# Performance work log

Measured on AMD Instinct MI355X. Metric: run time of the kernel, lower is better.

## Reference

```python
import jax, jax.numpy as jnp
import numpy as np

N = 40000          # nodes
E = 640000         # edges (before self-loops)
G = 64             # graphs
EMBED_DIM = 128
GAT_HIDDEN = 64    # per-head channels for g1/g2
GAT_OUT_DIM = 64   # per-head channels for g3 (concat=False)
HEADS = (4, 4, 4)
NEG_SLOPE = 0.2


def setup_inputs() -> dict:
    key = jax.random.key(0)
    ks = jax.random.split(key, 16)
    x = jax.random.normal(ks[0], (N, EMBED_DIM), dtype=jnp.float32)
    edge_index = jax.random.randint(ks[1], (2, E), 0, N, dtype=jnp.int64)
    batch = jnp.sort(jax.random.randint(ks[2], (N,), 0, G, dtype=jnp.int64))

    def lin(k, i, o):
        return jax.random.normal(k, (i, o), dtype=jnp.float32) * (1.0 / np.sqrt(i))

    H1, H2, H3 = HEADS
    d1_in, d1_out = EMBED_DIM, GAT_HIDDEN
    d2_in, d2_out = GAT_HIDDEN * H1, GAT_HIDDEN
    d3_in, d3_out = GAT_HIDDEN * H2, GAT_OUT_DIM
    params = dict(
        Wl1=lin(ks[3], d1_in, H1 * d1_out), Wr1=lin(ks[4], d1_in, H1 * d1_out),
        att1=jax.random.normal(ks[5], (H1, d1_out), dtype=jnp.float32) * 0.1,
        b1=jnp.zeros((H1 * d1_out,), jnp.float32),
        Wl2=lin(ks[6], d2_in, H2 * d2_out), Wr2=lin(ks[7], d2_in, H2 * d2_out),
        att2=jax.random.normal(ks[8], (H2, d2_out), dtype=jnp.float32) * 0.1,
        b2=jnp.zeros((H2 * d2_out,), jnp.float32),
        Wl3=lin(ks[9], d3_in, H3 * d3_out), Wr3=lin(ks[10], d3_in, H3 * d3_out),
        att3=jax.random.normal(ks[11], (H3, d3_out), dtype=jnp.float32) * 0.1,
        b3=jnp.zeros((d3_out,), jnp.float32),
        Wc=lin(ks[12], GAT_OUT_DIM, 2), bc=jnp.zeros((2,), jnp.float32),
    )
    return dict(x=x, edge_index=edge_index, batch=batch, **params)


def _gatv2(x, src, dst, Wl, Wr, att, bias, heads, out_c, concat):
    n = x.shape[0]
    xl = (x @ Wl).reshape(n, heads, out_c)   # source transform
    xr = (x @ Wr).reshape(n, heads, out_c)   # target transform
    # per-edge GATv2 score: att . LeakyReLU(xl[j] + xr[i])
    e = jax.nn.leaky_relu(xl[src] + xr[dst], NEG_SLOPE)      # [E,H,C]
    score = jnp.einsum('ehc,hc->eh', e, att)                  # [E,H]
    # segment softmax over incoming edges of each target node
    smax = jax.ops.segment_max(score, dst, num_segments=n)
    escore = jnp.exp(score - smax[dst])
    denom = jax.ops.segment_sum(escore, dst, num_segments=n)
    alpha = escore / (denom[dst] + 1e-16)                     # [E,H]
    out = jax.ops.segment_sum(alpha[:, :, None] * xl[src], dst, num_segments=n)
    out = out.reshape(n, heads * out_c) if concat else out.mean(axis=1)
    return out + bias


def reference(x, edge_index, batch, Wl1, Wr1, att1, b1, Wl2, Wr2, att2, b2,
              Wl3, Wr3, att3, b3, Wc, bc):
    n = x.shape[0]
    loops = jnp.arange(n, dtype=edge_index.dtype)
    src = jnp.concatenate([edge_index[0], loops])  # add self-loops (PyG default)
    dst = jnp.concatenate([edge_index[1], loops])
    act = lambda h: jax.nn.leaky_relu(h, NEG_SLOPE)
    h = act(_gatv2(x, src, dst, Wl1, Wr1, att1, b1, HEADS[0], GAT_HIDDEN, True))
    h = act(_gatv2(h, src, dst, Wl2, Wr2, att2, b2, HEADS[1], GAT_HIDDEN, True))
    h = _gatv2(h, src, dst, Wl3, Wr3, att3, b3, HEADS[2], GAT_OUT_DIM, False)
    g = jax.ops.segment_max(h, batch, num_segments=G)  # global_max_pool
    logits = g @ Wc + bc
    return logits, g
```

## Files before the change

### kernel.cpp

```cpp
#include <hip/hip_runtime.h>
#include <cstdint>

#define NN 40000
#define EE 640000
#define GG 64

typedef short bf16x8 __attribute__((ext_vector_type(8)));
typedef float f32x4 __attribute__((ext_vector_type(4)));

__device__ __forceinline__ float lrelu(float x) { return x > 0.f ? x : 0.2f * x; }

__device__ __forceinline__ unsigned short f2bf(float f) {
    unsigned u = __float_as_uint(f);
    return (unsigned short)((u + 0x7FFFu + ((u >> 16) & 1u)) >> 16);
}
__device__ __forceinline__ float bf2f(unsigned short h) {
    return __uint_as_float(((unsigned)h) << 16);
}

__device__ __forceinline__ unsigned fenc(float x) {
    unsigned u = __float_as_uint(x);
    return (u & 0x80000000u) ? ~u : (u | 0x80000000u);
}
__device__ __forceinline__ float fdec(unsigned e) {
    unsigned u = (e & 0x80000000u) ? (e ^ 0x80000000u) : ~e;
    return __uint_as_float(u);
}
#define ENC_NEG_INF 0x007FFFFFu

__device__ __forceinline__ void gload16(const void* g, void* l) {
    __builtin_amdgcn_global_load_lds(
        (const __attribute__((address_space(1))) unsigned int*)g,
        (__attribute__((address_space(3))) unsigned int*)l,
        16, 0, 0);
}

__global__ void k_init(int* deg, unsigned* gmax) {
    int i = blockIdx.x * blockDim.x + threadIdx.x;
    if (i < NN) deg[i] = 0;
    if (i < GG * 64) gmax[i] = ENC_NEG_INF;
}

__global__ void k_count(const int* __restrict__ dst, int* deg) {
    int e = blockIdx.x * blockDim.x + threadIdx.x;
    if (e < EE) atomicAdd(&deg[dst[e]], 1);
}

#define SCAN_T 1024
__global__ __launch_bounds__(SCAN_T) void k_scan(const int* __restrict__ deg,
                                                 int* row_ptr, int* cursor) {
    __shared__ int part[SCAN_T];
    const int t = threadIdx.x;
    const int CH = (NN + SCAN_T - 1) / SCAN_T;
    const int base = t * CH;
    int s = 0;
    for (int j = 0; j < CH; ++j) {
        int idx = base + j;
        if (idx < NN) s += deg[idx];
    }
    part[t] = s;
    __syncthreads();
    for (int off = 1; off < SCAN_T; off <<= 1) {
        int v = (t >= off) ? part[t - off] : 0;
        __syncthreads();
        part[t] += v;
        __syncthreads();
    }
    int run = (t == 0) ? 0 : part[t - 1];
    for (int j = 0; j < CH; ++j) {
        int idx = base + j;
        if (idx < NN) {
            row_ptr[idx] = run;
            cursor[idx]  = run;
            run += deg[idx];
        }
    }
    if (t == SCAN_T - 1) row_ptr[NN] = run;
}

__global__ void k_scatter(const int* __restrict__ src, const int* __restrict__ dst,
                          int* cursor, int* csr_src) {
    int e = blockIdx.x * blockDim.x + threadIdx.x;
    if (e < EE) {
        int p = atomicAdd(&cursor[dst[e]], 1);
        csr_src[p] = src[e];
    }
}

__global__ void k_xsplit(const float* __restrict__ x,
                         ushort* __restrict__ ah, ushort* __restrict__ am, int total4) {
    int i = blockIdx.x * blockDim.x + threadIdx.x;
    if (i >= total4) return;
    float4 v = ((const float4*)x)[i];
    ushort4 H, M;
    float* pv = &v.x;
    unsigned short* pH = &H.x; unsigned short* pM = &M.x;
#pragma unroll
    for (int j = 0; j < 4; ++j) {
        float a = pv[j];
        unsigned short h = f2bf(a);
        pH[j] = h;
        pM[j] = f2bf(a - bf2f(h));
    }
    ((ushort4*)ah)[i] = H;
    ((ushort4*)am)[i] = M;
}

__global__ __launch_bounds__(256) void k_wsplit(const float* __restrict__ W, int K,
                                                ushort* __restrict__ th,
                                                ushort* __restrict__ tm) {
    __shared__ float t[32][33];
    const int n0 = blockIdx.x * 32;
    const int k0 = blockIdx.y * 32;
    const int tx = threadIdx.x;
    const int ty = threadIdx.y;
#pragma unroll
    for (int i = 0; i < 4; ++i) {
        int kl = ty * 4 + i;
        t[kl][tx] = W[(size_t)(k0 + kl) * 256 + n0 + tx];
    }
    __syncthreads();
#pragma unroll
    for (int i = 0; i < 4; ++i) {
        int nl = ty * 4 + i;
        float a = t[tx][nl];
        unsigned short h = f2bf(a);
        size_t o = (size_t)(n0 + nl) * K + k0 + tx;
        th[o] = h;
        tm[o] = f2bf(a - bf2f(h));
    }
}

#define GBM 128
#define GBK 32
__global__ __launch_bounds__(256, 2) void gemm2(const ushort* __restrict__ Ah,
                                                const ushort* __restrict__ Am,
                                                const ushort* __restrict__ Bh,
                                                const ushort* __restrict__ Bm,
                                                float* __restrict__ C,
                                                int M, int K) {
    __shared__ ushort sAh[GBM * GBK];
    __shared__ ushort sAm[GBM * GBK];
    __shared__ ushort sBh[GBM * GBK];
    __shared__ ushort sBm[GBM * GBK];
    const int tid  = threadIdx.x;
    const int lane = tid & 63;
    const int wv   = tid >> 6;
    const int wm   = wv & 1;
    const int wn   = wv >> 1;
    const int bm   = blockIdx.x * GBM;
    const int bn   = blockIdx.y * 128;

    const ushort* gsrc = (wv == 0) ? Ah : (wv == 1) ? Am : (wv == 2) ? Bh : Bm;
    ushort* lbase = (wv == 0) ? sAh : (wv == 1) ? sAm : (wv == 2) ? sBh : sBm;
    const int rowbase = (wv < 2) ? bm : bn;

    f32x4 acc[4][4];
#pragma unroll
    for (int i = 0; i < 4; ++i)
#pragma unroll
        for (int j = 0; j < 4; ++j)
            acc[i][j] = (f32x4){0.f, 0.f, 0.f, 0.f};

    const int rl = lane >> 2;
    const int cs = lane & 3;
    const int fc = lane >> 4;
    const int fr = lane & 15;

    for (int k0 = 0; k0 < K; k0 += GBK) {
#pragma unroll
        for (int j = 0; j < 8; ++j) {
            const int lrow = j * 16 + rl;
            const int c    = cs ^ ((lrow >> 1) & 3);
            int grow = rowbase + lrow;
            grow = (grow >= M) ? (M - 1) : grow;
            gload16(gsrc + (size_t)grow * K + k0 + c * 8, lbase + j * 512);
        }
        __syncthreads();

        bf16x8 aH[4], aM[4], bH[4], bM[4];
#pragma unroll
        for (int mi = 0; mi < 4; ++mi) {
            const int row = wm * 64 + mi * 16 + fr;
            const int idx = row * 32 + (fc ^ ((row >> 1) & 3)) * 8;
            aH[mi] = *(const bf16x8*)&sAh[idx];
            aM[mi] = *(const bf16x8*)&sAm[idx];
        }
#pragma unroll
        for (int ni = 0; ni < 4; ++ni) {
            const int row = wn * 64 + ni * 16 + fr;
            const int idx = row * 32 + (fc ^ ((row >> 1) & 3)) * 8;
            bH[ni] = *(const bf16x8*)&sBh[idx];
            bM[ni] = *(const bf16x8*)&sBm[idx];
        }

#pragma unroll
        for (int mi = 0; mi < 4; ++mi)
#pragma unroll
            for (int ni = 0; ni < 4; ++ni) {
                f32x4 c0 = acc[mi][ni];
                c0 = __builtin_amdgcn_mfma_f32_16x16x32_bf16(aH[mi], bH[ni], c0, 0, 0, 0);
                c0 = __builtin_amdgcn_mfma_f32_16x16x32_bf16(aH[mi], bM[ni], c0, 0, 0, 0);
                c0 = __builtin_amdgcn_mfma_f32_16x16x32_bf16(aM[mi], bH[ni], c0, 0, 0, 0);
                acc[mi][ni] = c0;
            }
        __syncthreads();
    }

#pragma unroll
    for (int mi = 0; mi < 4; ++mi) {
#pragma unroll
        for (int r = 0; r < 4; ++r) {
            const int row = bm + wm * 64 + mi * 16 + (lane >> 4) * 4 + r;
            if (row < M) {
#pragma unroll
                for (int ni = 0; ni < 4; ++ni) {
                    const int col = bn + wn * 64 + ni * 16 + (lane & 15);
                    C[(size_t)row * 256 + col] = acc[mi][ni][r];
                }
            }
        }
    }
}

template <int MODE>
__global__ __launch_bounds__(256) void k_aggregate(const float* __restrict__ xl,
                                                   const float* __restrict__ xr,
                                                   const float* __restrict__ att,
                                                   const float* __restrict__ bias,
                                                   const int* __restrict__ row_ptr,
                                                   const int* __restrict__ csr_src,
                                                   ushort* __restrict__ oh,
                                                   ushort* __restrict__ om,
                                                   float* __restrict__ of) {
    const int wave = threadIdx.x >> 6;
    const int lane = threadIdx.x & 63;
    const int node = blockIdx.x * 4 + wave;
    if (node >= NN) return;

    const float4 xri = ((const float4*)(xr + (size_t)node * 256))[lane];
    const float4 av  = ((const float4*)att)[lane];

    float m = -INFINITY, d = 0.f;
    float a0 = 0.f, a1 = 0.f, a2 = 0.f, a3 = 0.f;

    const int start = row_ptr[node];
    const int endp  = row_ptr[node + 1];
    const int L = endp - start + 1;

    int i = 0;
    for (; i + 4 <= L; i += 4) {
        const int e0 = start + i;
        const int s0 = (e0     < endp) ? csr_src[e0]     : node;
        const int s1 = (e0 + 1 < endp) ? csr_src[e0 + 1] : node;
        const int s2 = (e0 + 2 < endp) ? csr_src[e0 + 2] : node;
        const int s3 = (e0 + 3 < endp) ? csr_src[e0 + 3] : node;
        const float4 x0 = ((const float4*)(xl + (size_t)s0 * 256))[lane];
        const float4 x1 = ((const float4*)(xl + (size_t)s1 * 256))[lane];
        const float4 x2 = ((const float4*)(xl + (size_t)s2 * 256))[lane];
        const float4 x3 = ((const float4*)(xl + (size_t)s3 * 256))[lane];
        float p0 = av.x * lrelu(x0.x + xri.x) + av.y * lrelu(x0.y + xri.y)
                 + av.z * lrelu(x0.z + xri.z) + av.w * lrelu(x0.w + xri.w);
        float p1 = av.x * lrelu(x1.x + xri.x) + av.y * lrelu(x1.y + xri.y)
                 + av.z * lrelu(x1.z + xri.z) + av.w * lrelu(x1.w + xri.w);
        float p2 = av.x * lrelu(x2.x + xri.x) + av.y * lrelu(x2.y + xri.y)
                 + av.z * lrelu(x2.z + xri.z) + av.w * lrelu(x2.w + xri.w);
        float p3 = av.x * lrelu(x3.x + xri.x) + av.y * lrelu(x3.y + xri.y)
                 + av.z * lrelu(x3.z + xri.z) + av.w * lrelu(x3.w + xri.w);
        p0 += __shfl_xor(p0, 1); p1 += __shfl_xor(p1, 1);
        p2 += __shfl_xor(p2, 1); p3 += __shfl_xor(p3, 1);
        p0 += __shfl_xor(p0, 2); p1 += __shfl_xor(p1, 2);
        p2 += __shfl_xor(p2, 2); p3 += __shfl_xor(p3, 2);
        p0 += __shfl_xor(p0, 4); p1 += __shfl_xor(p1, 4);
        p2 += __shfl_xor(p2, 4); p3 += __shfl_xor(p3, 4);
        p0 += __shfl_xor(p0, 8); p1 += __shfl_xor(p1, 8);
        p2 += __shfl_xor(p2, 8); p3 += __shfl_xor(p3, 8);

        const float pm = fmaxf(fmaxf(p0, p1), fmaxf(p2, p3));
        if (__all(pm <= m + 8.f)) {
            const float f0 = __expf(p0 - m), f1 = __expf(p1 - m);
            const float f2 = __expf(p2 - m), f3 = __expf(p3 - m);
            d  += f0 + f1 + f2 + f3;
            a0 += f0 * x0.x + f1 * x1.x + f2 * x2.x + f3 * x3.x;
            a1 += f0 * x0.y + f1 * x1.y + f2 * x2.y + f3 * x3.y;
            a2 += f0 * x0.z + f1 * x1.z + f2 * x2.z + f3 * x3.z;
            a3 += f0 * x0.w + f1 * x1.w + f2 * x2.w + f3 * x3.w;
        } else {
            const float mn = fmaxf(m, pm);
            const float sc = __expf(m - mn);
            const float f0 = __expf(p0 - mn), f1 = __expf(p1 - mn);
            const float f2 = __expf(p2 - mn), f3 = __expf(p3 - mn);
            d  = d  * sc + f0 + f1 + f2 + f3;
            a0 = a0 * sc + f0 * x0.x + f1 * x1.x + f2 * x2.x + f3 * x3.x;
            a1 = a1 * sc + f0 * x0.y + f1 * x1.y + f2 * x2.y + f3 * x3.y;
            a2 = a2 * sc + f0 * x0.z + f1 * x1.z + f2 * x2.z + f3 * x3.z;
            a3 = a3 * sc + f0 * x0.w + f1 * x1.w + f2 * x2.w + f3 * x3.w;
            m = mn;
        }
    }
    for (; i < L; ++i) {
        const int e0 = start + i;
        const int s0 = (e0 < endp) ? csr_src[e0] : node;
        const float4 x0 = ((const float4*)(xl + (size_t)s0 * 256))[lane];
        float p0 = av.x * lrelu(x0.x + xri.x) + av.y * lrelu(x0.y + xri.y)
                 + av.z * lrelu(x0.z + xri.z) + av.w * lrelu(x0.w + xri.w);
        p0 += __shfl_xor(p0, 1);
        p0 += __shfl_xor(p0, 2);
        p0 += __shfl_xor(p0, 4);
        p0 += __shfl_xor(p0, 8);
        if (__all(p0 <= m + 8.f)) {
            const float f0 = __expf(p0 - m);
            d += f0; a0 += f0 * x0.x; a1 += f0 * x0.y; a2 += f0 * x0.z; a3 += f0 * x0.w;
        } else {
            const float mn = fmaxf(m, p0);
            const float sc = __expf(m - mn);
            const float f0 = __expf(p0 - mn);
            d  = d  * sc + f0;
            a0 = a0 * sc + f0 * x0.x;
            a1 = a1 * sc + f0 * x0.y;
            a2 = a2 * sc + f0 * x0.z;
            a3 = a3 * sc + f0 * x0.w;
            m = mn;
        }
    }

    const float inv = 1.f / (d + 1e-16f);
    if (MODE == 0) {
        const int c = lane * 4;
        float v[4];
        v[0] = lrelu(a0 * inv + bias[c + 0]);
        v[1] = lrelu(a1 * inv + bias[c + 1]);
        v[2] = lrelu(a2 * inv + bias[c + 2]);
        v[3] = lrelu(a3 * inv + bias[c + 3]);
        ushort4 H, M4;
        unsigned short* pH = &H.x; unsigned short* pM = &M4.x;
#pragma unroll
        for (int j = 0; j < 4; ++j) {
            unsigned short h = f2bf(v[j]);
            pH[j] = h;
            pM[j] = f2bf(v[j] - bf2f(h));
        }
        const size_t o = (size_t)node * 64 + lane;
        ((ushort4*)oh)[o] = H;
        ((ushort4*)om)[o] = M4;
    } else {
        float v0 = a0 * inv, v1 = a1 * inv, v2 = a2 * inv, v3 = a3 * inv;
        v0 += __shfl_xor(v0, 16); v0 += __shfl_xor(v0, 32);
        v1 += __shfl_xor(v1, 16); v1 += __shfl_xor(v1, 32);
        v2 += __shfl_xor(v2, 16); v2 += __shfl_xor(v2, 32);
        v3 += __shfl_xor(v3, 16); v3 += __shfl_xor(v3, 32);
        if (lane < 16) {
            const int c = lane * 4;
            float4 o;
            o.x = v0 * 0.25f + bias[c + 0];
            o.y = v1 * 0.25f + bias[c + 1];
            o.z = v2 * 0.25f + bias[c + 2];
            o.w = v3 * 0.25f + bias[c + 3];
            ((float4*)(of + (size_t)node * 64))[lane] = o;
        }
    }
}

#define PNB 32
__global__ __launch_bounds__(64) void k_pool(const float* __restrict__ h3,
                                             const int* __restrict__ batch,
                                             unsigned* gmax) {
    const int lane = threadIdx.x;
    const int start = blockIdx.x * PNB;
    if (start >= NN) return;
    const int end = min(start + PNB, NN);
    int curg = batch[start];
    float best = -INFINITY;
    for (int n = start; n < end; ++n) {
        int g = batch[n];
        if (g != curg) {
            atomicMax(&gmax[curg * 64 + lane], fenc(best));
            best = -INFINITY;
            curg = g;
        }
        best = fmaxf(best, h3[(size_t)n * 64 + lane]);
    }
    atomicMax(&gmax[curg * 64 + lane], fenc(best));
}

__global__ void k_decode(const unsigned* __restrict__ gmax, float* __restrict__ outg) {
    int i = blockIdx.x * blockDim.x + threadIdx.x;
    if (i < GG * 64) outg[i] = fdec(gmax[i]);
}

__global__ __launch_bounds__(128) void k_head(const float* __restrict__ g,
                                              const float* __restrict__ Wc,
                                              const float* __restrict__ bc,
                                              float* __restrict__ logits) {
    const int t = threadIdx.x;
    const int gr = t >> 1, o = t & 1;
    float s = bc[o];
    for (int c = 0; c < 64; ++c) s = fmaf(g[gr * 64 + c], Wc[c * 2 + o], s);
    logits[t] = s;
}

extern "C" void kernel_launch(void* const* d_in, const int* in_sizes, int n_in,
                              void* d_out, int out_size, void* d_ws, size_t ws_size,
                              hipStream_t stream) {
    const float* x     = (const float*)d_in[0];
    const int*   ei    = (const int*)d_in[1];
    const int*   batch = (const int*)d_in[2];
    const float* Wl1 = (const float*)d_in[3];
    const float* Wr1 = (const float*)d_in[4];
    const float* att1 = (const float*)d_in[5];
    const float* b1  = (const float*)d_in[6];
    const float* Wl2 = (const float*)d_in[7];
    const float* Wr2 = (const float*)d_in[8];
    const float* att2 = (const float*)d_in[9];
    const float* b2  = (const float*)d_in[10];
    const float* Wl3 = (const float*)d_in[11];
    const float* Wr3 = (const float*)d_in[12];
    const float* att3 = (const float*)d_in[13];
    const float* b3  = (const float*)d_in[14];
    const float* Wc  = (const float*)d_in[15];
    const float* bc  = (const float*)d_in[16];
    float* out = (float*)d_out;

    char* ws = (char*)d_ws;
    size_t off = 0;
    auto alloc = [&](size_t bytes) -> void* {
        void* p = ws + off;
        off += (bytes + 255) & ~(size_t)255;
        return p;
    };
    float*  xlout = (float*)alloc((size_t)NN * 256 * 4);
    float*  xrout = (float*)alloc((size_t)NN * 256 * 4);
    ushort* Ah    = (ushort*)alloc((size_t)NN * 256 * 2);
    ushort* Am    = (ushort*)alloc((size_t)NN * 256 * 2);
    ushort* wt[6][2];
    for (int w = 0; w < 6; ++w)
        for (int s = 0; s < 2; ++s)
            wt[w][s] = (ushort*)alloc((size_t)256 * 256 * 2);
    int*   deg     = (int*)alloc((size_t)NN * 4);
    int*   cursor  = (int*)alloc((size_t)NN * 4);
    int*   row_ptr = (int*)alloc((size_t)(NN + 1) * 4);
    int*   csr_src = (int*)alloc((size_t)EE * 4);
    unsigned* gmax = (unsigned*)alloc((size_t)GG * 64 * 4);
    float* h3 = (float*)Ah;
    if (off > ws_size) return;

    const int* esrc = ei;
    const int* edst = ei + EE;

    k_init<<<(NN + 255) / 256, 256, 0, stream>>>(deg, gmax);
    k_count<<<(EE + 255) / 256, 256, 0, stream>>>(edst, deg);
    k_scan<<<1, SCAN_T, 0, stream>>>(deg, row_ptr, cursor);
    k_scatter<<<(EE + 255) / 256, 256, 0, stream>>>(esrc, edst, cursor, csr_src);

    k_xsplit<<<(NN * 128 / 4 + 255) / 256, 256, 0, stream>>>(x, Ah, Am, NN * 128 / 4);
    const float* Ws[6] = {Wl1, Wr1, Wl2, Wr2, Wl3, Wr3};
    const int    Ks[6] = {128, 128, 256, 256, 256, 256};
    for (int w = 0; w < 6; ++w) {
        dim3 g(8, Ks[w] / 32), b(32, 8);
        k_wsplit<<<g, b, 0, stream>>>(Ws[w], Ks[w], wt[w][0], wt[w][1]);
    }

    const dim3 gg((NN + GBM - 1) / GBM, 2);
    const int agg_blocks = NN / 4;

    gemm2<<<gg, 256, 0, stream>>>(Ah, Am, wt[0][0], wt[0][1], xlout, NN, 128);
    gemm2<<<gg, 256, 0, stream>>>(Ah, Am, wt[1][0], wt[1][1], xrout, NN, 128);
    k_aggregate<0><<<agg_blocks, 256, 0, stream>>>(xlout, xrout, att1, b1, row_ptr, csr_src,
                                                   Ah, Am, nullptr);
    gemm2<<<gg, 256, 0, stream>>>(Ah, Am, wt[2][0], wt[2][1], xlout, NN, 256);
    gemm2<<<gg, 256, 0, stream>>>(Ah, Am, wt[3][0], wt[3][1], xrout, NN, 256);
    k_aggregate<0><<<agg_blocks, 256, 0, stream>>>(xlout, xrout, att2, b2, row_ptr, csr_src,
                                                   Ah, Am, nullptr);
    gemm2<<<gg, 256, 0, stream>>>(Ah, Am, wt[4][0], wt[4][1], xlout, NN, 256);
    gemm2<<<gg, 256, 0, stream>>>(Ah, Am, wt[5][0], wt[5][1], xrout, NN, 256);
    k_aggregate<1><<<agg_blocks, 256, 0, stream>>>(xlout, xrout, att3, b3, row_ptr, csr_src,
                                                   nullptr, nullptr, h3);

    k_pool<<<(NN + PNB - 1) / PNB, 64, 0, stream>>>(h3, batch, gmax);
    k_decode<<<(GG * 64 + 255) / 256, 256, 0, stream>>>(gmax, out + 128);
    k_head<<<1, 128, 0, stream>>>(out + 128, Wc, bc, out);
}
```

Baseline: 721.2 us.

## Fuse left/right GAT projections into one GEMM with double-buffered LDS

Packs Wl and Wr of each layer into one 512-column weight, so a single GEMM produces an interleaved [N,512] xl|xr buffer. This halves the GEMM launches and reads the split activations once per layer instead of twice. The aggregation kernel now gathers source rows and its own target row from the interleaved buffer at a 512-float stride. The GEMM main loop also double-buffers its LDS tiles, prefetching the next K-tile while computing the current one. The cost is twice the shared memory per block, which may reduce occupancy.

```diff
diff --git a/kernel.cpp b/kernel.cpp
--- a/kernel.cpp
+++ b/kernel.cpp
@@ -106,7 +106,7 @@
     ((ushort4*)am)[i] = M;
 }
 
-__global__ __launch_bounds__(256) void k_wsplit(const float* __restrict__ W, int K,
+__global__ __launch_bounds__(256) void k_wsplit(const float* __restrict__ W, int K, int woff,
                                                 ushort* __restrict__ th,
                                                 ushort* __restrict__ tm) {
     __shared__ float t[32][33];
@@ -125,7 +125,7 @@
         int nl = ty * 4 + i;
         float a = t[tx][nl];
         unsigned short h = f2bf(a);
-        size_t o = (size_t)(n0 + nl) * K + k0 + tx;
+        size_t o = (size_t)(woff + n0 + nl) * K + k0 + tx;
         th[o] = h;
         tm[o] = f2bf(a - bf2f(h));
     }
@@ -133,16 +133,16 @@
 
 #define GBM 128
 #define GBK 32
-__global__ __launch_bounds__(256, 2) void gemm2(const ushort* __restrict__ Ah,
-                                                const ushort* __restrict__ Am,
-                                                const ushort* __restrict__ Bh,
-                                                const ushort* __restrict__ Bm,
-                                                float* __restrict__ C,
-                                                int M, int K) {
-    __shared__ ushort sAh[GBM * GBK];
-    __shared__ ushort sAm[GBM * GBK];
-    __shared__ ushort sBh[GBM * GBK];
-    __shared__ ushort sBm[GBM * GBK];
+__global__ __launch_bounds__(256, 2) void gemm2c(const ushort* __restrict__ Ah,
+                                                 const ushort* __restrict__ Am,
+                                                 const ushort* __restrict__ Bh,
+                                                 const ushort* __restrict__ Bm,
+                                                 float* __restrict__ C,
+                                                 int M, int K) {
+    __shared__ ushort sAh[2][GBM * GBK];
+    __shared__ ushort sAm[2][GBM * GBK];
+    __shared__ ushort sBh[2][GBM * GBK];
+    __shared__ ushort sBm[2][GBM * GBK];
     const int tid  = threadIdx.x;
     const int lane = tid & 63;
     const int wv   = tid >> 6;
@@ -152,7 +152,8 @@
     const int bn   = blockIdx.y * 128;
 
     const ushort* gsrc = (wv == 0) ? Ah : (wv == 1) ? Am : (wv == 2) ? Bh : Bm;
-    ushort* lbase = (wv == 0) ? sAh : (wv == 1) ? sAm : (wv == 2) ? sBh : sBm;
+    ushort* l0 = (wv == 0) ? sAh[0] : (wv == 1) ? sAm[0] : (wv == 2) ? sBh[0] : sBm[0];
+    ushort* l1 = (wv == 0) ? sAh[1] : (wv == 1) ? sAm[1] : (wv == 2) ? sBh[1] : sBm[1];
     const int rowbase = (wv < 2) ? bm : bn;
 
     f32x4 acc[4][4];
@@ -167,31 +168,45 @@
     const int fc = lane >> 4;
     const int fr = lane & 15;
 
-    for (int k0 = 0; k0 < K; k0 += GBK) {
+    auto stage = [&](ushort* lb, int kt) {
+        const int k0 = kt * GBK;
 #pragma unroll
         for (int j = 0; j < 8; ++j) {
             const int lrow = j * 16 + rl;
             const int c    = cs ^ ((lrow >> 1) & 3);
             int grow = rowbase + lrow;
             grow = (grow >= M) ? (M - 1) : grow;
-            gload16(gsrc + (size_t)grow * K + k0 + c * 8, lbase + j * 512);
-        }
-        __syncthreads();
+            gload16(gsrc + (size_t)grow * K + k0 + c * 8, lb + j * 512);
+        }
+    };
+
+    stage(l0, 0);
+    __syncthreads();
+
+    const int nt = K / GBK;
+    for (int t = 0; t < nt; ++t) {
+        if (t + 1 < nt) stage((t & 1) ? l0 : l1, t + 1);
+
+        const int b = t & 1;
+        const ushort* pAh = sAh[b];
+        const ushort* pAm = sAm[b];
+        const ushort* pBh = sBh[b];
+        const ushort* pBm = sBm[b];
 
         bf16x8 aH[4], aM[4], bH[4], bM[4];
 #pragma unroll
         for (int mi = 0; mi < 4; ++mi) {
             const int row = wm * 64 + mi * 16 + fr;
             const int idx = row * 32 + (fc ^ ((row >> 1) & 3)) * 8;
-            aH[mi] = *(const bf16x8*)&sAh[idx];
-            aM[mi] = *(const bf16x8*)&sAm[idx];
+            aH[mi] = *(const bf16x8*)&pAh[idx];
+            aM[mi] = *(const bf16x8*)&pAm[idx];
         }
 #pragma unroll
         for (int ni = 0; ni < 4; ++ni) {
             const int row = wn * 64 + ni * 16 + fr;
             const int idx = row * 32 + (fc ^ ((row >> 1) & 3)) * 8;
-            bH[ni] = *(const bf16x8*)&sBh[idx];
-            bM[ni] = *(const bf16x8*)&sBm[idx];
+            bH[ni] = *(const bf16x8*)&pBh[idx];
+            bM[ni] = *(const bf16x8*)&pBm[idx];
         }
 
 #pragma unroll
@@ -216,7 +231,7 @@
 #pragma unroll
                 for (int ni = 0; ni < 4; ++ni) {
                     const int col = bn + wn * 64 + ni * 16 + (lane & 15);
-                    C[(size_t)row * 256 + col] = acc[mi][ni][r];
+                    C[(size_t)row * 512 + col] = acc[mi][ni][r];
                 }
             }
         }
@@ -224,8 +239,7 @@
 }
 
 template <int MODE>
-__global__ __launch_bounds__(256) void k_aggregate(const float* __restrict__ xl,
-                                                   const float* __restrict__ xr,
+__global__ __launch_bounds__(256) void k_aggregate(const float* __restrict__ xlr,
                                                    const float* __restrict__ att,
                                                    const float* __restrict__ bias,
                                                    const int* __restrict__ row_ptr,
@@ -238,7 +252,7 @@
     const int node = blockIdx.x * 4 + wave;
     if (node >= NN) return;
 
-    const float4 xri = ((const float4*)(xr + (size_t)node * 256))[lane];
+    const float4 xri = ((const float4*)(xlr + (size_t)node * 512 + 256))[lane];
     const float4 av  = ((const float4*)att)[lane];
 
     float m = -INFINITY, d = 0.f;
@@ -255,10 +269,10 @@
         const int s1 = (e0 + 1 < endp) ? csr_src[e0 + 1] : node;
         const int s2 = (e0 + 2 < endp) ? csr_src[e0 + 2] : node;
         const int s3 = (e0 + 3 < endp) ? csr_src[e0 + 3] : node;
-        const float4 x0 = ((const float4*)(xl + (size_t)s0 * 256))[lane];
-        const float4 x1 = ((const float4*)(xl + (size_t)s1 * 256))[lane];
-        const float4 x2 = ((const float4*)(xl + (size_t)s2 * 256))[lane];
-        const float4 x3 = ((const float4*)(xl + (size_t)s3 * 256))[lane];
+        const float4 x0 = ((const float4*)(xlr + (size_t)s0 * 512))[lane];
+        const float4 x1 = ((const float4*)(xlr + (size_t)s1 * 512))[lane];
+        const float4 x2 = ((const float4*)(xlr + (size_t)s2 * 512))[lane];
+        const float4 x3 = ((const float4*)(xlr + (size_t)s3 * 512))[lane];
         float p0 = av.x * lrelu(x0.x + xri.x) + av.y * lrelu(x0.y + xri.y)
                  + av.z * lrelu(x0.z + xri.z) + av.w * lrelu(x0.w + xri.w);
         float p1 = av.x * lrelu(x1.x + xri.x) + av.y * lrelu(x1.y + xri.y)
@@ -301,7 +315,7 @@
     for (; i < L; ++i) {
         const int e0 = start + i;
         const int s0 = (e0 < endp) ? csr_src[e0] : node;
-        const float4 x0 = ((const float4*)(xl + (size_t)s0 * 256))[lane];
+        const float4 x0 = ((const float4*)(xlr + (size_t)s0 * 512))[lane];
         float p0 = av.x * lrelu(x0.x + xri.x) + av.y * lrelu(x0.y + xri.y)
                  + av.z * lrelu(x0.z + xri.z) + av.w * lrelu(x0.w + xri.w);
         p0 += __shfl_xor(p0, 1);
@@ -428,14 +442,14 @@
         off += (bytes + 255) & ~(size_t)255;
         return p;
     };
-    float*  xlout = (float*)alloc((size_t)NN * 256 * 4);
-    float*  xrout = (float*)alloc((size_t)NN * 256 * 4);
-    ushort* Ah    = (ushort*)alloc((size_t)NN * 256 * 2);
-    ushort* Am    = (ushort*)alloc((size_t)NN * 256 * 2);
-    ushort* wt[6][2];
-    for (int w = 0; w < 6; ++w)
+    float*  xlr = (float*)alloc((size_t)NN * 512 * 4);
+    ushort* Ah  = (ushort*)alloc((size_t)NN * 256 * 2);
+    ushort* Am  = (ushort*)alloc((size_t)NN * 256 * 2);
+    const int Ksz[3] = {128, 256, 256};
+    ushort* wtc[3][2];
+    for (int l = 0; l < 3; ++l)
         for (int s = 0; s < 2; ++s)
-            wt[w][s] = (ushort*)alloc((size_t)256 * 256 * 2);
+            wtc[l][s] = (ushort*)alloc((size_t)512 * Ksz[l] * 2);
     int*   deg     = (int*)alloc((size_t)NN * 4);
     int*   cursor  = (int*)alloc((size_t)NN * 4);
     int*   row_ptr = (int*)alloc((size_t)(NN + 1) * 4);
@@ -454,26 +468,23 @@
 
     k_xsplit<<<(NN * 128 / 4 + 255) / 256, 256, 0, stream>>>(x, Ah, Am, NN * 128 / 4);
     const float* Ws[6] = {Wl1, Wr1, Wl2, Wr2, Wl3, Wr3};
-    const int    Ks[6] = {128, 128, 256, 256, 256, 256};
     for (int w = 0; w < 6; ++w) {
-        dim3 g(8, Ks[w] / 32), b(32, 8);
-        k_wsplit<<<g, b, 0, stream>>>(Ws[w], Ks[w], wt[w][0], wt[w][1]);
-    }
-
-    const dim3 gg((NN + GBM - 1) / GBM, 2);
+        const int l = w >> 1, woff = (w & 1) * 256, K = Ksz[l];
+        dim3 g(8, K / 32), b(32, 8);
+        k_wsplit<<<g, b, 0, stream>>>(Ws[w], K, woff, wtc[l][0], wtc[l][1]);
+    }
+
+    const dim3 gg((NN + GBM - 1) / GBM, 4);
     const int agg_blocks = NN / 4;
 
-    gemm2<<<gg, 256, 0, stream>>>(Ah, Am, wt[0][0], wt[0][1], xlout, NN, 128);
-    gemm2<<<gg, 256, 0, stream>>>(Ah, Am, wt[1][0], wt[1][1], xrout, NN, 128);
-    k_aggregate<0><<<agg_blocks, 256, 0, stream>>>(xlout, xrout, att1, b1, row_ptr, csr_src,
+    gemm2c<<<gg, 256, 0, stream>>>(Ah, Am, wtc[0][0], wtc[0][1], xlr, NN, 128);
+    k_aggregate<0><<<agg_blocks, 256, 0, stream>>>(xlr, att1, b1, row_ptr, csr_src,
                                                    Ah, Am, nullptr);
-    gemm2<<<gg, 256, 0, stream>>>(Ah, Am, wt[2][0], wt[2][1], xlout, NN, 256);
-    gemm2<<<gg, 256, 0, stream>>>(Ah, Am, wt[3][0], wt[3][1], xrout, NN, 256);
-    k_aggregate<0><<<agg_blocks, 256, 0, stream>>>(xlout, xrout, att2, b2, row_ptr, csr_src,
+    gemm2c<<<gg, 256, 0, stream>>>(Ah, Am, wtc[1][0], wtc[1][1], xlr, NN, 256);
+    k_aggregate<0><<<agg_blocks, 256, 0, stream>>>(xlr, att2, b2, row_ptr, csr_src,
                                                    Ah, Am, nullptr);
-    gemm2<<<gg, 256, 0, stream>>>(Ah, Am, wt[4][0], wt[4][1], xlout, NN, 256);
-    gemm2<<<gg, 256, 0, stream>>>(Ah, Am, wt[5][0], wt[5][1], xrout, NN, 256);
-    k_aggregate<1><<<agg_blocks, 256, 0, stream>>>(xlout, xrout, att3, b3, row_ptr, csr_src,
+    gemm2c<<<gg, 256, 0, stream>>>(Ah, Am, wtc[2][0], wtc[2][1], xlr, NN, 256);
+    k_aggregate<1><<<agg_blocks, 256, 0, stream>>>(xlr, att3, b3, row_ptr, csr_src,
                                                    nullptr, nullptr, h3);
 
     k_pool<<<(NN + PNB - 1) / PNB, 64, 0, stream>>>(h3, batch, gmax);
```

Result: faster. 705.7 us (-2.1%).
